# Optimization experiments

Hardware: AMD Instinct MI355X
Metric: run time of the kernel (lower is better)

Reference implementation:

```python
import jax, jax.numpy as jnp
import numpy as np

N, E, D, D_OUT = 100000, 3200000, 64, 64
EPS = 1e-5


def setup_inputs() -> dict:
    key = jax.random.key(0)
    ks = jax.random.split(key, 16)
    s = 1.0 / np.sqrt(D)
    inp = {
        "x": jax.random.normal(ks[0], (N, D), dtype=jnp.float32),
        "edge_index": jax.random.randint(ks[1], (2, E), 0, N, dtype=jnp.int64),
        # layer 1: GCNConv weight/bias, fc weight/bias, BN gamma/beta
        "W1": jax.random.uniform(ks[2], (D, D), jnp.float32, -s, s),
        "b1": jnp.zeros((D,), jnp.float32),
        "fw1": jax.random.uniform(ks[3], (D, D), jnp.float32, -s, s),
        "fb1": jax.random.uniform(ks[4], (D,), jnp.float32, -s, s),
        "g1": jnp.ones((D,), jnp.float32),
        "bt1": jnp.zeros((D,), jnp.float32),
        # layer 2
        "W2": jax.random.uniform(ks[5], (D, D), jnp.float32, -s, s),
        "b2": jnp.zeros((D,), jnp.float32),
        "fw2": jax.random.uniform(ks[6], (D, D_OUT), jnp.float32, -s, s),
        "fb2": jax.random.uniform(ks[7], (D_OUT,), jnp.float32, -s, s),
        "g2": jnp.ones((D_OUT,), jnp.float32),
        "bt2": jnp.zeros((D_OUT,), jnp.float32),
    }
    return inp


def _gcn_conv(x, W, b, src, dst, dinv):
    # x' = X W, then symmetric-normalized scatter-add aggregation (self loops included)
    h = x @ W                                   # [N, D]
    msg = (dinv[src] * dinv[dst])[:, None] * h[src]  # [E+N, D]
    out = jax.ops.segment_sum(msg, dst, num_segments=N)
    return out + b


def _fc_bn_relu(x, fw, fb, g, bt):
    y = x @ fw + fb
    mu = jnp.mean(y, axis=0)
    var = jnp.mean((y - mu) ** 2, axis=0)  # biased var (torch BN training mode)
    y = (y - mu) * jax.lax.rsqrt(var + EPS) * g + bt
    return jax.nn.relu(y)


def reference(x, edge_index, W1, b1, fw1, fb1, g1, bt1, W2, b2, fw2, fb2, g2, bt2):
    loop = jnp.arange(N, dtype=edge_index.dtype)
    src = jnp.concatenate([edge_index[0], loop])  # add self loops
    dst = jnp.concatenate([edge_index[1], loop])
    deg = jax.ops.segment_sum(jnp.ones_like(dst, dtype=x.dtype), dst, num_segments=N)
    dinv = jax.lax.rsqrt(deg)  # deg >= 1 thanks to self loops

    h = _gcn_conv(x, W1, b1, src, dst, dinv)
    h = _fc_bn_relu(h, fw1, fb1, g1, bt1)
    h = _gcn_conv(h, W2, b2, src, dst, dinv)
    h = _fc_bn_relu(h, fw2, fb2, g2, bt2)
    return h
```

## Files before the change

### kernel.cpp

```cpp
#include <hip/hip_runtime.h>

#define N_NODES 100000
#define N_EDGES 3200000
#define D 64
#define EPS 1e-5f

#define BSHIFT 7
#define BNODES 128
#define NBUCK ((N_NODES + BNODES - 1) / BNODES)
#define P1_CHUNK 4096
#define NB_P1 ((N_EDGES + P1_CHUNK - 1) / P1_CHUNK)
#define SRC_MASK 0x1FFFFu
#define BCAP 4480
#define TBL_STRIDE 784

typedef _Float16 f16x8 __attribute__((ext_vector_type(8)));
typedef _Float16 half2v __attribute__((ext_vector_type(2)));
typedef unsigned int u32x4 __attribute__((ext_vector_type(4)));
typedef __attribute__((ext_vector_type(4))) float f32x4;

__device__ __forceinline__ unsigned short f2h(float f) {
  return __builtin_bit_cast(unsigned short, (_Float16)f);
}
__device__ __forceinline__ half2v u2h(unsigned int u) {
  return __builtin_bit_cast(half2v, u);
}
__device__ __forceinline__ unsigned int h2u(half2v h) {
  return __builtin_bit_cast(unsigned int, h);
}
__device__ __forceinline__ float2 hpair(unsigned int u) {
  half2v h = __builtin_bit_cast(half2v, u);
  return make_float2((float)h.x, (float)h.y);
}
__device__ __forceinline__ void addp(half2v a[4], uint4 u) {
  a[0] += u2h(u.x);
  a[1] += u2h(u.y);
  a[2] += u2h(u.z);
  a[3] += u2h(u.w);
}

__global__ __launch_bounds__(256) void combine_weights(
    const float* __restrict__ W1, const float* __restrict__ b1,
    const float* __restrict__ fw1, const float* __restrict__ fb1,
    const float* __restrict__ W2, const float* __restrict__ b2,
    const float* __restrict__ fw2, const float* __restrict__ fb2,
    unsigned int* __restrict__ WcB1, float* __restrict__ bc1,
    unsigned int* __restrict__ WcB2, float* __restrict__ bc2,
    float* __restrict__ stats) {
  if (blockIdx.x == 2) {
    if (threadIdx.x < 256) stats[threadIdx.x] = 0.0f;
    return;
  }
  const float* W  = blockIdx.x ? W2  : W1;
  const float* fw = blockIdx.x ? fw2 : fw1;
  const float* b  = blockIdx.x ? b2  : b1;
  const float* fb = blockIdx.x ? fb2 : fb1;
  unsigned int* WcB = blockIdx.x ? WcB2 : WcB1;
  float* bc = blockIdx.x ? bc2 : bc1;

  __shared__ float sW[64 * 64];
  __shared__ float sf[64 * 64];
  __shared__ float sC[64 * 64];
  for (int i = threadIdx.x; i < 4096; i += 256) { sW[i] = W[i]; sf[i] = fw[i]; }
  __syncthreads();
  for (int o = threadIdx.x; o < 4096; o += 256) {
    int i = o >> 6, j = o & 63;
    float acc = 0.f;
    #pragma unroll
    for (int k = 0; k < 64; ++k) acc += sW[i * 64 + k] * sf[k * 64 + j];
    sC[o] = acc;
  }
  __syncthreads();
  for (int o = threadIdx.x; o < 2048; o += 256) {
    int jj = o & 3, L = (o >> 2) & 63, kh = (o >> 8) & 1, nt = o >> 9;
    int k0 = (L >> 4) * 8 + jj * 2 + kh * 32;
    int n  = nt * 16 + (L & 15);
    unsigned int lo = f2h(sC[k0 * 64 + n]);
    unsigned int hi = f2h(sC[(k0 + 1) * 64 + n]);
    WcB[o] = (hi << 16) | lo;
  }
  if (threadIdx.x < 64) {
    int j = threadIdx.x;
    float acc = fb[j];
    #pragma unroll
    for (int k = 0; k < 64; ++k) acc += b[k] * sf[k * 64 + j];
    bc[j] = acc;
  }
}

__global__ __launch_bounds__(256) void pass1_sort(
    const int* __restrict__ src, const int* __restrict__ dst,
    unsigned int* __restrict__ stage, unsigned short* __restrict__ tbl) {
  __shared__ unsigned int hist[NBUCK];
  __shared__ unsigned int ts[256];
  __shared__ unsigned int sorted[P1_CHUNK];
  const int tid = threadIdx.x;
  const int e0 = blockIdx.x * P1_CHUNK;

  for (int b = tid; b < NBUCK; b += 256) hist[b] = 0;
  __syncthreads();

  int dreg[16];
  #pragma unroll
  for (int k = 0; k < 16; ++k) {
    int e = e0 + k * 256 + tid;
    int d = (e < N_EDGES) ? dst[e] : -1;
    dreg[k] = d;
    if (d >= 0) atomicAdd(&hist[((unsigned)d) >> BSHIFT], 1u);
  }
  __syncthreads();

  unsigned int v[4], run = 0;
  #pragma unroll
  for (int j = 0; j < 4; ++j) {
    int bk = 4 * tid + j;
    unsigned int h = (bk < NBUCK) ? hist[bk] : 0u;
    v[j] = run;
    run += h;
  }
  ts[tid] = run;
  __syncthreads();
  for (int o = 1; o < 256; o <<= 1) {
    unsigned int add = (tid >= o) ? ts[tid - o] : 0u;
    __syncthreads();
    ts[tid] += add;
    __syncthreads();
  }
  const unsigned int excl = ts[tid] - run;
  const unsigned int m = ts[255];
  unsigned short* trow = tbl + (size_t)blockIdx.x * TBL_STRIDE;
  #pragma unroll
  for (int j = 0; j < 4; ++j) {
    int bk = 4 * tid + j;
    if (bk < NBUCK) {
      unsigned int o = excl + v[j];
      hist[bk] = o;
      trow[bk] = (unsigned short)o;
    }
  }
  if (tid == 0) trow[NBUCK] = (unsigned short)m;
  __syncthreads();

  #pragma unroll
  for (int k = 0; k < 16; ++k) {
    int e = e0 + k * 256 + tid;
    int t = dreg[k];
    if (t >= 0) {
      unsigned int pos = atomicAdd(&hist[((unsigned)t) >> BSHIFT], 1u);
      sorted[pos] = (((unsigned)(t & (BNODES - 1))) << 17) | (unsigned)src[e];
    }
  }
  __syncthreads();

  unsigned int* so = stage + (size_t)blockIdx.x * P1_CHUNK;
  for (int i = tid; i < (int)m; i += 256) so[i] = sorted[i];
}

__global__ __launch_bounds__(512) void pass2_sort(
    const unsigned int* __restrict__ stage, const unsigned short* __restrict__ tbl,
    int* __restrict__ eSrc, int* __restrict__ off, int* __restrict__ edeg,
    float* __restrict__ dinv, const float* __restrict__ x,
    unsigned short* __restrict__ Xs) {
  __shared__ int spre[512];
  __shared__ int cnt[BNODES];
  __shared__ int ts[BNODES];
  __shared__ float dinvL[BNODES];
  __shared__ unsigned int raw[BCAP];
  __shared__ int sorted[BCAP];
  const int b = blockIdx.x, tid = threadIdx.x;
  const int n0 = b * BNODES;

  int base0 = 0, base1 = 0, len0 = 0, len1 = 0;
  {
    int s0 = 2 * tid, s1 = 2 * tid + 1;
    if (s0 < NB_P1) {
      const unsigned short* trow = tbl + (size_t)s0 * TBL_STRIDE;
      int o0 = trow[b], o1 = trow[b + 1];
      base0 = s0 * P1_CHUNK + o0;
      len0 = o1 - o0;
    }
    if (s1 < NB_P1) {
      const unsigned short* trow = tbl + (size_t)s1 * TBL_STRIDE;
      int o0 = trow[b], o1 = trow[b + 1];
      base1 = s1 * P1_CHUNK + o0;
      len1 = o1 - o0;
    }
  }
  if (tid < BNODES) cnt[tid] = 0;
  const int mylen = len0 + len1;
  spre[tid] = mylen;
  __syncthreads();
  for (int o = 1; o < 512; o <<= 1) {
    int add = (tid >= o) ? spre[tid - o] : 0;
    __syncthreads();
    spre[tid] += add;
    __syncthreads();
  }
  const int m = spre[511];
  const int pref = spre[tid] - mylen;

  for (int j = 0; j < len0; ++j) {
    unsigned int p = stage[base0 + j];
    raw[pref + j] = p;
    atomicAdd(&cnt[p >> 17], 1);
  }
  for (int j = 0; j < len1; ++j) {
    unsigned int p = stage[base1 + j];
    raw[pref + len0 + j] = p;
    atomicAdd(&cnt[p >> 17], 1);
  }
  __syncthreads();

  int v = 0;
  if (tid < BNODES) { v = cnt[tid]; ts[tid] = v; }
  __syncthreads();
  for (int o = 1; o < BNODES; o <<= 1) {
    int add = (tid >= o && tid < BNODES) ? ts[tid - o] : 0;
    __syncthreads();
    if (tid < BNODES) ts[tid] += add;
    __syncthreads();
  }
  if (tid < BNODES) {
    int excl = ts[tid] - v;
    int node = n0 + tid;
    float dv = rsqrtf((float)v + 1.0f);
    dinvL[tid] = dv;
    if (node < N_NODES) {
      off[node]  = b * BCAP + excl;
      edeg[node] = v;
      dinv[node] = dv;
    }
    cnt[tid] = excl;
  }
  __syncthreads();

  for (int i = tid; i < m; i += 512) {
    unsigned int p = raw[i];
    int pos = atomicAdd(&cnt[p >> 17], 1);
    if (pos < BCAP) sorted[pos] = (int)(p & SRC_MASK);
  }
  __syncthreads();

  int* out = eSrc + (size_t)b * BCAP;
  for (int i = tid; i < m; i += 512) out[i] = sorted[i];

  const int rows = min(BNODES, N_NODES - n0);
  for (int i = tid; i < rows * 64; i += 512) {
    int r = i >> 6;
    size_t g = (size_t)(n0 + r) * 64 + (i & 63);
    Xs[g] = f2h(dinvL[r] * x[g]);
  }
}

__global__ __launch_bounds__(256) void agg_csr(
    const int* __restrict__ off, const int* __restrict__ edeg,
    const int* __restrict__ eSrc, const unsigned short* __restrict__ Xs,
    const float* __restrict__ dinv, unsigned short* __restrict__ agg) {
  const int wid = (blockIdx.x * 256 + threadIdx.x) >> 6;
  const int lane = threadIdx.x & 63;
  const int grp = lane >> 3, sub = lane & 7;
  if (wid >= N_NODES) return;
  const int s0 = off[wid];
  const int s1 = s0 + edeg[wid];
  const uint4* XsV = (const uint4*)Xs;

  half2v acc[4];
  {
    uint4 u = XsV[(size_t)wid * 8 + sub];
    if (grp != 0) { u.x = 0; u.y = 0; u.z = 0; u.w = 0; }
    acc[0] = u2h(u.x);
    acc[1] = u2h(u.y);
    acc[2] = u2h(u.z);
    acc[3] = u2h(u.w);
  }

  int e = s0;
  const int eend = s1 - ((s1 - s0) & 31);
  for (; e < eend; e += 32) {
    int sa = __builtin_nontemporal_load(&eSrc[e + grp]);
    int sb = __builtin_nontemporal_load(&eSrc[e + 8 + grp]);
    int sc = __builtin_nontemporal_load(&eSrc[e + 16 + grp]);
    int sd = __builtin_nontemporal_load(&eSrc[e + 24 + grp]);
    uint4 ua = XsV[(size_t)sa * 8 + sub];
    uint4 ub = XsV[(size_t)sb * 8 + sub];
    uint4 uc = XsV[(size_t)sc * 8 + sub];
    uint4 ud = XsV[(size_t)sd * 8 + sub];
    addp(acc, ua); addp(acc, ub); addp(acc, uc); addp(acc, ud);
  }
  if (e < s1) {
    const int lim = s1 - 1;
    int ea = e + grp, eb = e + 8 + grp, ec = e + 16 + grp, ed = e + 24 + grp;
    int sa = __builtin_nontemporal_load(&eSrc[min(ea, lim)]);
    int sb = __builtin_nontemporal_load(&eSrc[min(eb, lim)]);
    int sc = __builtin_nontemporal_load(&eSrc[min(ec, lim)]);
    int sd = __builtin_nontemporal_load(&eSrc[min(ed, lim)]);
    uint4 ua = XsV[(size_t)sa * 8 + sub];
    uint4 ub = XsV[(size_t)sb * 8 + sub];
    uint4 uc = XsV[(size_t)sc * 8 + sub];
    uint4 ud = XsV[(size_t)sd * 8 + sub];
    if (ea > lim) { ua.x = 0; ua.y = 0; ua.z = 0; ua.w = 0; }
    if (eb > lim) { ub.x = 0; ub.y = 0; ub.z = 0; ub.w = 0; }
    if (ec > lim) { uc.x = 0; uc.y = 0; uc.z = 0; uc.w = 0; }
    if (ed > lim) { ud.x = 0; ud.y = 0; ud.z = 0; ud.w = 0; }
    addp(acc, ua); addp(acc, ub); addp(acc, uc); addp(acc, ud);
  }

  #pragma unroll
  for (int mk = 8; mk <= 32; mk <<= 1) {
    #pragma unroll
    for (int i = 0; i < 4; ++i)
      acc[i] += u2h(__shfl_xor(h2u(acc[i]), mk, 64));
  }

  if (grp == 0) {
    _Float16 dh = (_Float16)dinv[wid];
    half2v d2 = {dh, dh};
    u32x4 o;
    o.x = h2u(acc[0] * d2);
    o.y = h2u(acc[1] * d2);
    o.z = h2u(acc[2] * d2);
    o.w = h2u(acc[3] * d2);
    __builtin_nontemporal_store(o, (u32x4*)(agg + (size_t)wid * 64 + sub * 8));
  }
}

__global__ __launch_bounds__(256) void gemm_stats(
    const unsigned short* __restrict__ A, const unsigned int* __restrict__ WcB,
    const float* __restrict__ bc, unsigned short* __restrict__ Yb,
    float* __restrict__ colsum, float* __restrict__ colsq) {
  const int tid = threadIdx.x;
  const int L = tid & 63, wv = tid >> 6;
  const int quad = L >> 4, l16 = L & 15;

  const f16x8* Wv = (const f16x8*)WcB;
  f16x8 bfr[4][2];
  #pragma unroll
  for (int nt = 0; nt < 4; ++nt)
    #pragma unroll
    for (int kh = 0; kh < 2; ++kh)
      bfr[nt][kh] = Wv[(nt * 2 + kh) * 64 + L];
  float bcv[4];
  #pragma unroll
  for (int nt = 0; nt < 4; ++nt) bcv[nt] = bc[nt * 16 + l16];

  const f16x8* Av = (const f16x8*)A;
  float psum[4] = {0.f, 0.f, 0.f, 0.f}, psq[4] = {0.f, 0.f, 0.f, 0.f};

  #pragma unroll
  for (int loop = 0; loop < 2; ++loop) {
    const int rowbase = blockIdx.x * 128 + loop * 64 + wv * 16;
    const int m = min(rowbase + l16, N_NODES - 1);
    f16x8 a0 = Av[(size_t)m * 8 + quad];
    f16x8 a1 = Av[(size_t)m * 8 + 4 + quad];
    #pragma unroll
    for (int nt = 0; nt < 4; ++nt) {
      f32x4 acc = {0.f, 0.f, 0.f, 0.f};
      acc = __builtin_amdgcn_mfma_f32_16x16x32_f16(a0, bfr[nt][0], acc, 0, 0, 0);
      acc = __builtin_amdgcn_mfma_f32_16x16x32_f16(a1, bfr[nt][1], acc, 0, 0, 0);
      #pragma unroll
      for (int r = 0; r < 4; ++r) {
        int row = rowbase + quad * 4 + r;
        if (row < N_NODES) {
          float y = acc[r] + bcv[nt];
          Yb[(size_t)row * 64 + nt * 16 + l16] = f2h(y);
          psum[nt] += y;
          psq[nt] += y * y;
        }
      }
    }
  }

  #pragma unroll
  for (int nt = 0; nt < 4; ++nt) {
    psum[nt] += __shfl_xor(psum[nt], 16, 64);
    psum[nt] += __shfl_xor(psum[nt], 32, 64);
    psq[nt]  += __shfl_xor(psq[nt], 16, 64);
    psq[nt]  += __shfl_xor(psq[nt], 32, 64);
  }
  __shared__ float rsum[4][64];
  __shared__ float rsq[4][64];
  if (L < 16) {
    #pragma unroll
    for (int nt = 0; nt < 4; ++nt) {
      rsum[wv][nt * 16 + L] = psum[nt];
      rsq[wv][nt * 16 + L]  = psq[nt];
    }
  }
  __syncthreads();
  if (tid < 64) {
    float s = rsum[0][tid] + rsum[1][tid] + rsum[2][tid] + rsum[3][tid];
    float q = rsq[0][tid] + rsq[1][tid] + rsq[2][tid] + rsq[3][tid];
    atomicAdd(&colsum[tid], s);
    atomicAdd(&colsq[tid], q);
  }
}

__global__ __launch_bounds__(256) void prescale_y(
    unsigned short* __restrict__ YbXs, const float* __restrict__ dinv,
    const float* __restrict__ colsum, const float* __restrict__ colsq,
    const float* __restrict__ g, const float* __restrict__ bt) {
  __shared__ float sa[64], sc[64];
  if (threadIdx.x < 64) {
    int j = threadIdx.x;
    float mu = colsum[j] * (1.0f / N_NODES);
    float var = colsq[j] * (1.0f / N_NODES) - mu * mu;
    float s = rsqrtf(var + EPS) * g[j];
    sa[j] = s;
    sc[j] = bt[j] - mu * s;
  }
  __syncthreads();
  int idx = blockIdx.x * blockDim.x + threadIdx.x;
  if (idx < N_NODES * 8) {
    int r = idx >> 3, c0 = (idx & 7) * 8;
    float dv = dinv[r];
    uint4 u = ((const uint4*)YbXs)[idx];
    float2 p0 = hpair(u.x), p1 = hpair(u.y), p2 = hpair(u.z), p3 = hpair(u.w);
    p0.x = dv * fmaxf(fmaf(p0.x, sa[c0    ], sc[c0    ]), 0.f);
    p0.y = dv * fmaxf(fmaf(p0.y, sa[c0 + 1], sc[c0 + 1]), 0.f);
    p1.x = dv * fmaxf(fmaf(p1.x, sa[c0 + 2], sc[c0 + 2]), 0.f);
    p1.y = dv * fmaxf(fmaf(p1.y, sa[c0 + 3], sc[c0 + 3]), 0.f);
    p2.x = dv * fmaxf(fmaf(p2.x, sa[c0 + 4], sc[c0 + 4]), 0.f);
    p2.y = dv * fmaxf(fmaf(p2.y, sa[c0 + 5], sc[c0 + 5]), 0.f);
    p3.x = dv * fmaxf(fmaf(p3.x, sa[c0 + 6], sc[c0 + 6]), 0.f);
    p3.y = dv * fmaxf(fmaf(p3.y, sa[c0 + 7], sc[c0 + 7]), 0.f);
    uint4 o;
    o.x = ((unsigned)f2h(p0.y) << 16) | f2h(p0.x);
    o.y = ((unsigned)f2h(p1.y) << 16) | f2h(p1.x);
    o.z = ((unsigned)f2h(p2.y) << 16) | f2h(p2.x);
    o.w = ((unsigned)f2h(p3.y) << 16) | f2h(p3.x);
    ((uint4*)YbXs)[idx] = o;
  }
}

__global__ __launch_bounds__(256) void final_norm(
    const unsigned short* __restrict__ Yb, float* __restrict__ out,
    const float* __restrict__ colsum, const float* __restrict__ colsq,
    const float* __restrict__ g, const float* __restrict__ bt) {
  __shared__ float sa[64], sc[64];
  if (threadIdx.x < 64) {
    int j = threadIdx.x;
    float mu = colsum[j] * (1.0f / N_NODES);
    float var = colsq[j] * (1.0f / N_NODES) - mu * mu;
    float s = rsqrtf(var + EPS) * g[j];
    sa[j] = s;
    sc[j] = bt[j] - mu * s;
  }
  __syncthreads();
  int idx = blockIdx.x * blockDim.x + threadIdx.x;
  if (idx < N_NODES * 8) {
    int c0 = (idx & 7) * 8;
    uint4 u = ((const uint4*)Yb)[idx];
    float2 p0 = hpair(u.x), p1 = hpair(u.y), p2 = hpair(u.z), p3 = hpair(u.w);
    float4 o0, o1;
    o0.x = fmaxf(fmaf(p0.x, sa[c0    ], sc[c0    ]), 0.f);
    o0.y = fmaxf(fmaf(p0.y, sa[c0 + 1], sc[c0 + 1]), 0.f);
    o0.z = fmaxf(fmaf(p1.x, sa[c0 + 2], sc[c0 + 2]), 0.f);
    o0.w = fmaxf(fmaf(p1.y, sa[c0 + 3], sc[c0 + 3]), 0.f);
    o1.x = fmaxf(fmaf(p2.x, sa[c0 + 4], sc[c0 + 4]), 0.f);
    o1.y = fmaxf(fmaf(p2.y, sa[c0 + 5], sc[c0 + 5]), 0.f);
    o1.z = fmaxf(fmaf(p3.x, sa[c0 + 6], sc[c0 + 6]), 0.f);
    o1.w = fmaxf(fmaf(p3.y, sa[c0 + 7], sc[c0 + 7]), 0.f);
    ((float4*)out)[idx * 2] = o0;
    ((float4*)out)[idx * 2 + 1] = o1;
  }
}

extern "C" void kernel_launch(void* const* d_in, const int* in_sizes, int n_in,
                              void* d_out, int out_size, void* d_ws, size_t ws_size,
                              hipStream_t stream) {
  const float* x   = (const float*)d_in[0];
  const int*   src = (const int*)d_in[1];
  const int*   dst = src + N_EDGES;
  const float* W1  = (const float*)d_in[2];
  const float* b1  = (const float*)d_in[3];
  const float* fw1 = (const float*)d_in[4];
  const float* fb1 = (const float*)d_in[5];
  const float* g1  = (const float*)d_in[6];
  const float* bt1 = (const float*)d_in[7];
  const float* W2  = (const float*)d_in[8];
  const float* b2  = (const float*)d_in[9];
  const float* fw2 = (const float*)d_in[10];
  const float* fb2 = (const float*)d_in[11];
  const float* g2  = (const float*)d_in[12];
  const float* bt2 = (const float*)d_in[13];

  float* out = (float*)d_out;

  unsigned char* w = (unsigned char*)d_ws;
  unsigned int*   stage = (unsigned int*)w;
  unsigned short* aggb  = (unsigned short*)w;
  size_t ofs = ((size_t)NB_P1 * P1_CHUNK * 4 + 255) & ~(size_t)255;
  float*          dinv  = (float*)(w + ofs);
  unsigned short* XsYb  = (unsigned short*)(dinv + N_NODES);
  int*            eSrc  = (int*)(XsYb + (size_t)N_NODES * D);
  int*            off   = eSrc + (size_t)NBUCK * BCAP;
  int*            edeg  = off + N_NODES;
  unsigned short* tbl   = (unsigned short*)(edeg + N_NODES);
  unsigned int* WcB1 = (unsigned int*)(tbl + (size_t)NB_P1 * TBL_STRIDE);
  float* bc1  = (float*)(WcB1 + 2048);
  unsigned int* WcB2 = (unsigned int*)(bc1 + 64);
  float* bc2  = (float*)(WcB2 + 2048);
  float* sum1 = bc2 + 64;
  float* sq1  = sum1 + 64;
  float* sum2 = sq1 + 64;
  float* sq2  = sum2 + 64;

  const int nd = N_NODES * D;
  const int nv = N_NODES * 8;
  dim3 blk(256);

  combine_weights<<<3, blk, 0, stream>>>(W1, b1, fw1, fb1, W2, b2, fw2, fb2,
                                         WcB1, bc1, WcB2, bc2, sum1);
  pass1_sort<<<NB_P1, blk, 0, stream>>>(src, dst, stage, tbl);
  pass2_sort<<<NBUCK, 512, 0, stream>>>(stage, tbl, eSrc, off, edeg, dinv, x, XsYb);
  agg_csr<<<(nd + 255) / 256, blk, 0, stream>>>(off, edeg, eSrc, XsYb, dinv, aggb);
  gemm_stats<<<(N_NODES + 127) / 128, blk, 0, stream>>>(aggb, WcB1, bc1, XsYb, sum1, sq1);
  prescale_y<<<(nv + 255) / 256, blk, 0, stream>>>(XsYb, dinv, sum1, sq1, g1, bt1);
  agg_csr<<<(nd + 255) / 256, blk, 0, stream>>>(off, edeg, eSrc, XsYb, dinv, aggb);
  gemm_stats<<<(N_NODES + 127) / 128, blk, 0, stream>>>(aggb, WcB2, bc2, XsYb, sum2, sq2);
  final_norm<<<(nv + 255) / 256, blk, 0, stream>>>(XsYb, out, sum2, sq2, g2, bt2);
}
```

Measured before the change: 332.4 us.

## Process two nodes per wavefront in CSR aggregation with shuffled edge indices

The aggregation kernel now assigns two destination nodes per 64-lane wavefront, each handled by 32 lanes, so only four edges are gathered in parallel per node instead of eight. Each half loads up to 32 source indices in a single coalesced load and broadcasts them with shuffles, then issues eight independent feature gathers before accumulating. High-degree nodes fall back to a slower loop of four edges at a time. The aim is to cut idle lanes on average-degree nodes (about 33 edges) and the serialised index-load latency, at the cost of more register pressure and a reduction tree shortened to two shuffle steps.

```diff
diff --git a/kernel.cpp b/kernel.cpp
--- a/kernel.cpp
+++ b/kernel.cpp
@@ -256,71 +256,76 @@
     const int* __restrict__ off, const int* __restrict__ edeg,
     const int* __restrict__ eSrc, const unsigned short* __restrict__ Xs,
     const float* __restrict__ dinv, unsigned short* __restrict__ agg) {
-  const int wid = (blockIdx.x * 256 + threadIdx.x) >> 6;
+  const int wv = (blockIdx.x * 256 + threadIdx.x) >> 6;
   const int lane = threadIdx.x & 63;
-  const int grp = lane >> 3, sub = lane & 7;
-  if (wid >= N_NODES) return;
-  const int s0 = off[wid];
-  const int s1 = s0 + edeg[wid];
+  const int half = lane >> 5;
+  const int l32 = lane & 31;
+  const int grp = l32 >> 3;
+  const int sub = lane & 7;
+  const int node = wv * 2 + half;
+  if (node >= N_NODES) return;
+
+  const int s0 = off[node];
+  const int deg = edeg[node];
+  const float dvf = dinv[node];
   const uint4* XsV = (const uint4*)Xs;
+
+  int eidx = node;
+  if (deg > 0) {
+    int li = (l32 < deg) ? l32 : deg - 1;
+    eidx = __builtin_nontemporal_load(&eSrc[s0 + li]);
+  }
 
   half2v acc[4];
   {
-    uint4 u = XsV[(size_t)wid * 8 + sub];
-    if (grp != 0) { u.x = 0; u.y = 0; u.z = 0; u.w = 0; }
+    uint4 u = XsV[(size_t)node * 8 + sub];
+    if (l32 >= 8) { u.x = 0; u.y = 0; u.z = 0; u.w = 0; }
     acc[0] = u2h(u.x);
     acc[1] = u2h(u.y);
     acc[2] = u2h(u.z);
     acc[3] = u2h(u.w);
   }
 
-  int e = s0;
-  const int eend = s1 - ((s1 - s0) & 31);
-  for (; e < eend; e += 32) {
-    int sa = __builtin_nontemporal_load(&eSrc[e + grp]);
-    int sb = __builtin_nontemporal_load(&eSrc[e + 8 + grp]);
-    int sc = __builtin_nontemporal_load(&eSrc[e + 16 + grp]);
-    int sd = __builtin_nontemporal_load(&eSrc[e + 24 + grp]);
-    uint4 ua = XsV[(size_t)sa * 8 + sub];
-    uint4 ub = XsV[(size_t)sb * 8 + sub];
-    uint4 uc = XsV[(size_t)sc * 8 + sub];
-    uint4 ud = XsV[(size_t)sd * 8 + sub];
-    addp(acc, ua); addp(acc, ub); addp(acc, uc); addp(acc, ud);
-  }
-  if (e < s1) {
-    const int lim = s1 - 1;
-    int ea = e + grp, eb = e + 8 + grp, ec = e + 16 + grp, ed = e + 24 + grp;
-    int sa = __builtin_nontemporal_load(&eSrc[min(ea, lim)]);
-    int sb = __builtin_nontemporal_load(&eSrc[min(eb, lim)]);
-    int sc = __builtin_nontemporal_load(&eSrc[min(ec, lim)]);
-    int sd = __builtin_nontemporal_load(&eSrc[min(ed, lim)]);
-    uint4 ua = XsV[(size_t)sa * 8 + sub];
-    uint4 ub = XsV[(size_t)sb * 8 + sub];
-    uint4 uc = XsV[(size_t)sc * 8 + sub];
-    uint4 ud = XsV[(size_t)sd * 8 + sub];
-    if (ea > lim) { ua.x = 0; ua.y = 0; ua.z = 0; ua.w = 0; }
-    if (eb > lim) { ub.x = 0; ub.y = 0; ub.z = 0; ub.w = 0; }
-    if (ec > lim) { uc.x = 0; uc.y = 0; uc.z = 0; uc.w = 0; }
-    if (ed > lim) { ud.x = 0; ud.y = 0; ud.z = 0; ud.w = 0; }
-    addp(acc, ua); addp(acc, ub); addp(acc, uc); addp(acc, ud);
-  }
-
-  #pragma unroll
-  for (int mk = 8; mk <= 32; mk <<= 1) {
+  uint4 g[8];
+  #pragma unroll
+  for (int j = 0; j < 8; ++j) {
+    int srcn = __shfl(eidx, half * 32 + j * 4 + grp, 64);
+    g[j] = XsV[(size_t)srcn * 8 + sub];
+  }
+  #pragma unroll
+  for (int j = 0; j < 8; ++j) {
+    uint4 u = g[j];
+    if (j * 4 + grp >= deg) { u.x = 0; u.y = 0; u.z = 0; u.w = 0; }
+    addp(acc, u);
+  }
+
+  if (deg > 32) {
+    const int lim = deg - 1;
+    for (int e = 32; e < deg; e += 4) {
+      int ee = e + grp;
+      int srcn = __builtin_nontemporal_load(&eSrc[s0 + min(ee, lim)]);
+      uint4 u = XsV[(size_t)srcn * 8 + sub];
+      if (ee > lim) { u.x = 0; u.y = 0; u.z = 0; u.w = 0; }
+      addp(acc, u);
+    }
+  }
+
+  #pragma unroll
+  for (int mk = 8; mk <= 16; mk <<= 1) {
     #pragma unroll
     for (int i = 0; i < 4; ++i)
       acc[i] += u2h(__shfl_xor(h2u(acc[i]), mk, 64));
   }
 
-  if (grp == 0) {
-    _Float16 dh = (_Float16)dinv[wid];
+  if (l32 < 8) {
+    _Float16 dh = (_Float16)dvf;
     half2v d2 = {dh, dh};
     u32x4 o;
     o.x = h2u(acc[0] * d2);
     o.y = h2u(acc[1] * d2);
     o.z = h2u(acc[2] * d2);
     o.w = h2u(acc[3] * d2);
-    __builtin_nontemporal_store(o, (u32x4*)(agg + (size_t)wid * 64 + sub * 8));
+    __builtin_nontemporal_store(o, (u32x4*)(agg + (size_t)node * 64 + sub * 8));
   }
 }
 
@@ -505,18 +510,18 @@
   float* sum2 = sq1 + 64;
   float* sq2  = sum2 + 64;
 
-  const int nd = N_NODES * D;
   const int nv = N_NODES * 8;
+  const int nagg = (N_NODES + 7) / 8;
   dim3 blk(256);
 
   combine_weights<<<3, blk, 0, stream>>>(W1, b1, fw1, fb1, W2, b2, fw2, fb2,
                                          WcB1, bc1, WcB2, bc2, sum1);
   pass1_sort<<<NB_P1, blk, 0, stream>>>(src, dst, stage, tbl);
   pass2_sort<<<NBUCK, 512, 0, stream>>>(stage, tbl, eSrc, off, edeg, dinv, x, XsYb);
-  agg_csr<<<(nd + 255) / 256, blk, 0, stream>>>(off, edeg, eSrc, XsYb, dinv, aggb);
+  agg_csr<<<nagg, blk, 0, stream>>>(off, edeg, eSrc, XsYb, dinv, aggb);
   gemm_stats<<<(N_NODES + 127) / 128, blk, 0, stream>>>(aggb, WcB1, bc1, XsYb, sum1, sq1);
   prescale_y<<<(nv + 255) / 256, blk, 0, stream>>>(XsYb, dinv, sum1, sq1, g1, bt1);
-  agg_csr<<<(nd + 255) / 256, blk, 0, stream>>>(off, edeg, eSrc, XsYb, dinv, aggb);
+  agg_csr<<<nagg, blk, 0, stream>>>(off, edeg, eSrc, XsYb, dinv, aggb);
   gemm_stats<<<(N_NODES + 127) / 128, blk, 0, stream>>>(aggb, WcB2, bc2, XsYb, sum2, sq2);
   final_norm<<<(nv + 255) / 256, blk, 0, stream>>>(XsYb, out, sum2, sq2, g2, bt2);
 }
```

After: 328.0 us. Within noise of the previous version (-1.3%).
